# Kernel optimization log

Hardware: AMD Instinct MI355X
Metric: run time of the kernel (lower is better)

Reference implementation:

```python
import jax, jax.numpy as jnp
import numpy as np

N_PARTIAL = 1024  # matches init_kwargs


def setup_inputs() -> dict:
    key = jax.random.key(0)
    k1, k2 = jax.random.split(key)
    B, H, L = 8, 768, 4096
    x = jax.random.normal(k1, (B, H, L), dtype=jnp.float32)
    k = jax.random.normal(k2, (H, L), dtype=jnp.float32)
    return {"x": x, "k": k}


def reference(x, k):
    # FFT-based causal long convolution with low-pass frequency truncation.
    L = x.shape[-1]
    N = 2 * L  # zero-pad to 2L for linear (non-circular) convolution
    x_dtype = x.dtype
    x_f = jnp.fft.rfft(x.astype(jnp.float32), n=N)          # [B, H, N//2+1] complex64
    k_f = jnp.fft.rfft(k.astype(jnp.float32), n=N)          # [H, N//2+1]   complex64
    # zero out all frequency bins >= N_partial // 2 (low-pass truncation of the kernel)
    freqs = jnp.arange(N // 2 + 1)
    k_f = jnp.where(freqs < N_PARTIAL // 2, k_f, jnp.zeros((), dtype=k_f.dtype))
    y_f = x_f * k_f                                          # broadcast over batch
    y = jnp.fft.irfft(y_f, n=N)[..., :L].astype(x_dtype)     # [B, H, L]
    return y
```

## Files before the change

### kernel.cpp

```cpp
#include <hip/hip_runtime.h>
#include <math.h>

#define LSEQ 4096
#define NFFT 8192
#define NF   512
#define NF2  1024
#define NH   768
#define NBH  6144
#define MROWS 6912

typedef __attribute__((ext_vector_type(8))) short short8;
typedef __attribute__((ext_vector_type(4))) float floatx4;

__device__ __forceinline__ unsigned short f2bf(float f) {
    unsigned int u = __float_as_uint(f);
    u += 0x7fff + ((u >> 16) & 1);
    return (unsigned short)(u >> 16);
}

__device__ __forceinline__ void gld16(const unsigned short* g, unsigned short* l) {
    __builtin_amdgcn_global_load_lds(
        (const __attribute__((address_space(1))) void*)g,
        (__attribute__((address_space(3))) void*)l, 16, 0, 0);
}

__global__ void build_tables(unsigned short* __restrict__ T1,
                             unsigned short* __restrict__ T2) {
    __shared__ unsigned short tile[64][66];
    const int t = threadIdx.x;
    const int F0 = blockIdx.x * 64;
    const int N0 = blockIdx.y * 64;
#pragma unroll
    for (int i = 0; i < 16; ++i) {
        int r = (t >> 6) + i * 4;
        int c = t & 63;
        int f2 = F0 + r, n = N0 + c;
        int f = f2 >> 1;
        int p = (f * n) & (NFFT - 1);
        float th = (float)p * (float)(2.0 * M_PI / (double)NFFT);
        float s, cc;
        sincosf(th, &s, &cc);
        unsigned short v = f2bf((f2 & 1) ? s : cc);
        T1[(size_t)f2 * LSEQ + n] = v;
        tile[r][c] = v;
    }
    __syncthreads();
#pragma unroll
    for (int i = 0; i < 16; ++i) {
        int r = (t >> 6) + i * 4;
        int c = t & 63;
        T2[(size_t)(N0 + r) * NF2 + F0 + c] = tile[c][r];
    }
}

__global__ void tobf16(const float* __restrict__ x, const float* __restrict__ kk,
                       unsigned short* __restrict__ o) {
    size_t e = ((size_t)blockIdx.x * 256 + threadIdx.x) * 4;
    const size_t XN = (size_t)NBH * LSEQ;
    const float* s = (e < XN) ? (x + e) : (kk + (e - XN));
    float4 v = *(const float4*)s;
    unsigned int lo = (unsigned int)f2bf(v.x) | ((unsigned int)f2bf(v.y) << 16);
    unsigned int hi = (unsigned int)f2bf(v.z) | ((unsigned int)f2bf(v.w) << 16);
    *(uint2*)(o + e) = make_uint2(lo, hi);
}

__global__ __launch_bounds__(256) void gemm_bt(
    const unsigned short* __restrict__ A,
    const unsigned short* __restrict__ B,
    float* __restrict__ C,
    int M, int N, int K)
{
    __shared__ __align__(16) unsigned short As[2][128 * 32];
    __shared__ __align__(16) unsigned short Bs[2][128 * 32];
    const int t = threadIdx.x;
    const int w = t >> 6, l = t & 63;
    const int m0 = blockIdx.y * 128, n0 = blockIdx.x * 128;
    const int wm = (w >> 1) * 64, wn = (w & 1) * 64;
    const int lq = l >> 4, lr = l & 15;

    floatx4 acc[4][4];
#pragma unroll
    for (int i = 0; i < 4; ++i)
#pragma unroll
        for (int j = 0; j < 4; ++j)
            acc[i][j] = (floatx4){0.f, 0.f, 0.f, 0.f};

    const int sr = l >> 2, se = (l & 3) * 8;
    const int c0 = 2 * w, c1 = 2 * w + 1;
    const unsigned short* gA0 = A + (size_t)(m0 + c0 * 16 + sr) * K + se;
    const unsigned short* gA1 = A + (size_t)(m0 + c1 * 16 + sr) * K + se;
    const unsigned short* gB0 = B + (size_t)(n0 + c0 * 16 + sr) * K + se;
    const unsigned short* gB1 = B + (size_t)(n0 + c1 * 16 + sr) * K + se;

    gld16(gA0, As[0] + c0 * 512);
    gld16(gA1, As[0] + c1 * 512);
    gld16(gB0, Bs[0] + c0 * 512);
    gld16(gB1, Bs[0] + c1 * 512);
    __syncthreads();

    int cur = 0;
    for (int k0 = 32; k0 < K; k0 += 32) {
        const int nxt = cur ^ 1;
        gld16(gA0 + k0, As[nxt] + c0 * 512);
        gld16(gA1 + k0, As[nxt] + c1 * 512);
        gld16(gB0 + k0, Bs[nxt] + c0 * 512);
        gld16(gB1 + k0, Bs[nxt] + c1 * 512);

        short8 af[4], bfv[4];
#pragma unroll
        for (int i = 0; i < 4; ++i)
            af[i] = *(const short8*)(As[cur] + (wm + 16 * i + lr) * 32 + lq * 8);
#pragma unroll
        for (int j = 0; j < 4; ++j)
            bfv[j] = *(const short8*)(Bs[cur] + (wn + 16 * j + lr) * 32 + lq * 8);
#pragma unroll
        for (int i = 0; i < 4; ++i)
#pragma unroll
            for (int j = 0; j < 4; ++j)
                acc[i][j] = __builtin_amdgcn_mfma_f32_16x16x32_bf16(af[i], bfv[j], acc[i][j], 0, 0, 0);

        __syncthreads();
        cur = nxt;
    }

    {
        short8 af[4], bfv[4];
#pragma unroll
        for (int i = 0; i < 4; ++i)
            af[i] = *(const short8*)(As[cur] + (wm + 16 * i + lr) * 32 + lq * 8);
#pragma unroll
        for (int j = 0; j < 4; ++j)
            bfv[j] = *(const short8*)(Bs[cur] + (wn + 16 * j + lr) * 32 + lq * 8);
#pragma unroll
        for (int i = 0; i < 4; ++i)
#pragma unroll
            for (int j = 0; j < 4; ++j)
                acc[i][j] = __builtin_amdgcn_mfma_f32_16x16x32_bf16(af[i], bfv[j], acc[i][j], 0, 0, 0);
    }

#pragma unroll
    for (int i = 0; i < 4; ++i)
#pragma unroll
        for (int j = 0; j < 4; ++j)
#pragma unroll
            for (int r = 0; r < 4; ++r) {
                int row = m0 + wm + 16 * i + lq * 4 + r;
                int col = n0 + wn + 16 * j + lr;
                C[(size_t)row * N + col] = acc[i][j][r];
            }
}

__global__ void combine(const float* __restrict__ C1, unsigned short* __restrict__ AB) {
    int idx = blockIdx.x * blockDim.x + threadIdx.x;
    int bh = idx >> 9;
    int f = idx & (NF - 1);
    int h = bh % NH;
    const float* xc = C1 + (size_t)bh * NF2 + 2 * f;
    const float* kc = C1 + (size_t)(NBH + h) * NF2 + 2 * f;
    float Xre = xc[0], Xim = -xc[1];
    float Kre = kc[0], Kim = -kc[1];
    float s = (f == 0 ? 1.0f : 2.0f) * (1.0f / (float)NFFT);
    float Av = s * (Xre * Kre - Xim * Kim);
    float Bv = -(s * (Xre * Kim + Xim * Kre));
    unsigned int packed = (unsigned int)f2bf(Av) | ((unsigned int)f2bf(Bv) << 16);
    *(unsigned int*)(AB + (size_t)bh * NF2 + 2 * f) = packed;
}

extern "C" void kernel_launch(void* const* d_in, const int* in_sizes, int n_in,
                              void* d_out, int out_size, void* d_ws, size_t ws_size,
                              hipStream_t stream) {
    const float* x = (const float*)d_in[0];
    const float* k = (const float*)d_in[1];
    float* y = (float*)d_out;

    unsigned short* T1 = (unsigned short*)d_ws;
    unsigned short* T2 = T1 + (size_t)NF2 * LSEQ;
    unsigned short* AB = T2 + (size_t)LSEQ * NF2;

    unsigned short* Abm = (unsigned short*)d_out;
    float* C1 = (float*)((char*)d_out + (size_t)MROWS * LSEQ * 2);

    const int blk = 256;
    hipLaunchKernelGGL(build_tables, dim3(NF2 / 64, LSEQ / 64), dim3(blk), 0, stream, T1, T2);
    hipLaunchKernelGGL(tobf16, dim3((MROWS * LSEQ / 4) / blk), dim3(blk), 0, stream, x, k, Abm);
    hipLaunchKernelGGL(gemm_bt, dim3(NF2 / 128, MROWS / 128), dim3(blk), 0, stream,
                       Abm, T1, C1, MROWS, NF2, LSEQ);
    hipLaunchKernelGGL(combine, dim3((NBH * NF) / blk), dim3(blk), 0, stream, C1, AB);
    hipLaunchKernelGGL(gemm_bt, dim3(LSEQ / 128, NBH / 128), dim3(blk), 0, stream,
                       AB, T2, y, NBH, LSEQ, NF2);
}
```

Before: 356.6 us.

## Split-K the forward DFT GEMM and switch to register-staged double buffering

```diff
diff --git a/kernel.cpp b/kernel.cpp
--- a/kernel.cpp
+++ b/kernel.cpp
@@ -8,6 +8,7 @@
 #define NH   768
 #define NBH  6144
 #define MROWS 6912
+#define SPLIT_ROW 3456
 
 typedef __attribute__((ext_vector_type(8))) short short8;
 typedef __attribute__((ext_vector_type(4))) float floatx4;
@@ -16,12 +17,6 @@
     unsigned int u = __float_as_uint(f);
     u += 0x7fff + ((u >> 16) & 1);
     return (unsigned short)(u >> 16);
-}
-
-__device__ __forceinline__ void gld16(const unsigned short* g, unsigned short* l) {
-    __builtin_amdgcn_global_load_lds(
-        (const __attribute__((address_space(1))) void*)g,
-        (__attribute__((address_space(3))) void*)l, 16, 0, 0);
 }
 
 __global__ void build_tables(unsigned short* __restrict__ T1,
@@ -64,11 +59,42 @@
     *(uint2*)(o + e) = make_uint2(lo, hi);
 }
 
+#define LOADSET(ra0, ra1, rb0, rb1, off)                      \
+    ra0 = *(const uint4*)(pa0 + (off));                        \
+    ra1 = *(const uint4*)(pa1 + (off));                        \
+    rb0 = *(const uint4*)(pb0 + (off));                        \
+    rb1 = *(const uint4*)(pb1 + (off));
+
+#define WRITESET(buf, ra0, ra1, rb0, rb1)                      \
+    *(uint4*)(As[buf] + q0 * 8) = ra0;                         \
+    *(uint4*)(As[buf] + q1 * 8) = ra1;                         \
+    *(uint4*)(Bs[buf] + q0 * 8) = rb0;                         \
+    *(uint4*)(Bs[buf] + q1 * 8) = rb1;
+
+#define COMPUTE(buf)                                                          \
+    {                                                                         \
+        short8 af[4], bfv[4];                                                 \
+        _Pragma("unroll")                                                     \
+        for (int i = 0; i < 4; ++i)                                           \
+            af[i] = *(const short8*)(As[buf] + (wm + 16 * i + lr) * 32 + lq * 8); \
+        _Pragma("unroll")                                                     \
+        for (int j = 0; j < 4; ++j)                                           \
+            bfv[j] = *(const short8*)(Bs[buf] + (wn + 16 * j + lr) * 32 + lq * 8); \
+        _Pragma("unroll")                                                     \
+        for (int i = 0; i < 4; ++i)                                           \
+            _Pragma("unroll")                                                 \
+            for (int j = 0; j < 4; ++j)                                       \
+                acc[i][j] = __builtin_amdgcn_mfma_f32_16x16x32_bf16(          \
+                    af[i], bfv[j], acc[i][j], 0, 0, 0);                       \
+    }
+
 __global__ __launch_bounds__(256) void gemm_bt(
     const unsigned short* __restrict__ A,
     const unsigned short* __restrict__ B,
     float* __restrict__ C,
-    int M, int N, int K)
+    float* __restrict__ P1a,
+    float* __restrict__ P1b,
+    int M, int N, int ldk, int Ksub)
 {
     __shared__ __align__(16) unsigned short As[2][128 * 32];
     __shared__ __align__(16) unsigned short Bs[2][128 * 32];
@@ -77,6 +103,7 @@
     const int m0 = blockIdx.y * 128, n0 = blockIdx.x * 128;
     const int wm = (w >> 1) * 64, wn = (w & 1) * 64;
     const int lq = l >> 4, lr = l & 15;
+    const int kbase = blockIdx.z * Ksub;
 
     floatx4 acc[4][4];
 #pragma unroll
@@ -85,59 +112,44 @@
         for (int j = 0; j < 4; ++j)
             acc[i][j] = (floatx4){0.f, 0.f, 0.f, 0.f};
 
-    const int sr = l >> 2, se = (l & 3) * 8;
-    const int c0 = 2 * w, c1 = 2 * w + 1;
-    const unsigned short* gA0 = A + (size_t)(m0 + c0 * 16 + sr) * K + se;
-    const unsigned short* gA1 = A + (size_t)(m0 + c1 * 16 + sr) * K + se;
-    const unsigned short* gB0 = B + (size_t)(n0 + c0 * 16 + sr) * K + se;
-    const unsigned short* gB1 = B + (size_t)(n0 + c1 * 16 + sr) * K + se;
-
-    gld16(gA0, As[0] + c0 * 512);
-    gld16(gA1, As[0] + c1 * 512);
-    gld16(gB0, Bs[0] + c0 * 512);
-    gld16(gB1, Bs[0] + c1 * 512);
+    const int q0 = t, q1 = t + 256;
+    const int r0 = q0 >> 2, e0 = (q0 & 3) * 8;
+    const int r1 = q1 >> 2, e1 = (q1 & 3) * 8;
+    const unsigned short* pa0 = A + (size_t)(m0 + r0) * ldk + e0 + kbase;
+    const unsigned short* pa1 = A + (size_t)(m0 + r1) * ldk + e1 + kbase;
+    const unsigned short* pb0 = B + (size_t)(n0 + r0) * ldk + e0 + kbase;
+    const unsigned short* pb1 = B + (size_t)(n0 + r1) * ldk + e1 + kbase;
+
+    uint4 xa0, xa1, xb0, xb1;
+    uint4 ya0, ya1, yb0, yb1;
+
+    LOADSET(xa0, xa1, xb0, xb1, 0)
+    WRITESET(0, xa0, xa1, xb0, xb1)
+    LOADSET(ya0, ya1, yb0, yb1, 32)
     __syncthreads();
 
-    int cur = 0;
-    for (int k0 = 32; k0 < K; k0 += 32) {
-        const int nxt = cur ^ 1;
-        gld16(gA0 + k0, As[nxt] + c0 * 512);
-        gld16(gA1 + k0, As[nxt] + c1 * 512);
-        gld16(gB0 + k0, Bs[nxt] + c0 * 512);
-        gld16(gB1 + k0, Bs[nxt] + c1 * 512);
-
-        short8 af[4], bfv[4];
-#pragma unroll
-        for (int i = 0; i < 4; ++i)
-            af[i] = *(const short8*)(As[cur] + (wm + 16 * i + lr) * 32 + lq * 8);
-#pragma unroll
-        for (int j = 0; j < 4; ++j)
-            bfv[j] = *(const short8*)(Bs[cur] + (wn + 16 * j + lr) * 32 + lq * 8);
-#pragma unroll
-        for (int i = 0; i < 4; ++i)
-#pragma unroll
-            for (int j = 0; j < 4; ++j)
-                acc[i][j] = __builtin_amdgcn_mfma_f32_16x16x32_bf16(af[i], bfv[j], acc[i][j], 0, 0, 0);
-
+    const int T = Ksub >> 5;
+    for (int tt = 0; tt + 4 <= T; tt += 2) {
+        LOADSET(xa0, xa1, xb0, xb1, (tt + 2) * 32)
+        COMPUTE(0)
+        WRITESET(1, ya0, ya1, yb0, yb1)
         __syncthreads();
-        cur = nxt;
-    }
-
-    {
-        short8 af[4], bfv[4];
-#pragma unroll
-        for (int i = 0; i < 4; ++i)
-            af[i] = *(const short8*)(As[cur] + (wm + 16 * i + lr) * 32 + lq * 8);
-#pragma unroll
-        for (int j = 0; j < 4; ++j)
-            bfv[j] = *(const short8*)(Bs[cur] + (wn + 16 * j + lr) * 32 + lq * 8);
-#pragma unroll
-        for (int i = 0; i < 4; ++i)
-#pragma unroll
-            for (int j = 0; j < 4; ++j)
-                acc[i][j] = __builtin_amdgcn_mfma_f32_16x16x32_bf16(af[i], bfv[j], acc[i][j], 0, 0, 0);
-    }
-
+        LOADSET(ya0, ya1, yb0, yb1, (tt + 3) * 32)
+        COMPUTE(1)
+        WRITESET(0, xa0, xa1, xb0, xb1)
+        __syncthreads();
+    }
+    COMPUTE(0)
+    WRITESET(1, ya0, ya1, yb0, yb1)
+    __syncthreads();
+    COMPUTE(1)
+
+    float* Cb;
+    if (blockIdx.z == 0) {
+        Cb = C;
+    } else {
+        Cb = (m0 < SPLIT_ROW) ? P1a : (P1b - (size_t)SPLIT_ROW * N);
+    }
 #pragma unroll
     for (int i = 0; i < 4; ++i)
 #pragma unroll
@@ -146,19 +158,27 @@
             for (int r = 0; r < 4; ++r) {
                 int row = m0 + wm + 16 * i + lq * 4 + r;
                 int col = n0 + wn + 16 * j + lr;
-                C[(size_t)row * N + col] = acc[i][j][r];
+                Cb[(size_t)row * N + col] = acc[i][j][r];
             }
 }
 
-__global__ void combine(const float* __restrict__ C1, unsigned short* __restrict__ AB) {
+__global__ void combine(const float* __restrict__ C1,
+                        const float* __restrict__ P1a,
+                        const float* __restrict__ P1b,
+                        unsigned short* __restrict__ AB) {
     int idx = blockIdx.x * blockDim.x + threadIdx.x;
     int bh = idx >> 9;
     int f = idx & (NF - 1);
     int h = bh % NH;
     const float* xc = C1 + (size_t)bh * NF2 + 2 * f;
-    const float* kc = C1 + (size_t)(NBH + h) * NF2 + 2 * f;
-    float Xre = xc[0], Xim = -xc[1];
-    float Kre = kc[0], Kim = -kc[1];
+    const float* xp = (bh < SPLIT_ROW)
+        ? (P1a + (size_t)bh * NF2 + 2 * f)
+        : (P1b + (size_t)(bh - SPLIT_ROW) * NF2 + 2 * f);
+    const int kr = NBH + h;
+    const float* kc = C1 + (size_t)kr * NF2 + 2 * f;
+    const float* kp = P1b + (size_t)(kr - SPLIT_ROW) * NF2 + 2 * f;
+    float Xre = xc[0] + xp[0], Xim = -(xc[1] + xp[1]);
+    float Kre = kc[0] + kp[0], Kim = -(kc[1] + kp[1]);
     float s = (f == 0 ? 1.0f : 2.0f) * (1.0f / (float)NFFT);
     float Av = s * (Xre * Kre - Xim * Kim);
     float Bv = -(s * (Xre * Kim + Xim * Kre));
@@ -176,16 +196,18 @@
     unsigned short* T1 = (unsigned short*)d_ws;
     unsigned short* T2 = T1 + (size_t)NF2 * LSEQ;
     unsigned short* AB = T2 + (size_t)LSEQ * NF2;
+    float* P1a = (float*)(AB + (size_t)NBH * NF2);
 
     unsigned short* Abm = (unsigned short*)d_out;
     float* C1 = (float*)((char*)d_out + (size_t)MROWS * LSEQ * 2);
+    float* P1b = C1 + (size_t)MROWS * NF2;
 
     const int blk = 256;
     hipLaunchKernelGGL(build_tables, dim3(NF2 / 64, LSEQ / 64), dim3(blk), 0, stream, T1, T2);
     hipLaunchKernelGGL(tobf16, dim3((MROWS * LSEQ / 4) / blk), dim3(blk), 0, stream, x, k, Abm);
-    hipLaunchKernelGGL(gemm_bt, dim3(NF2 / 128, MROWS / 128), dim3(blk), 0, stream,
-                       Abm, T1, C1, MROWS, NF2, LSEQ);
-    hipLaunchKernelGGL(combine, dim3((NBH * NF) / blk), dim3(blk), 0, stream, C1, AB);
-    hipLaunchKernelGGL(gemm_bt, dim3(LSEQ / 128, NBH / 128), dim3(blk), 0, stream,
-                       AB, T2, y, NBH, LSEQ, NF2);
-}
+    hipLaunchKernelGGL(gemm_bt, dim3(NF2 / 128, MROWS / 128, 2), dim3(blk), 0, stream,
+                       Abm, T1, C1, P1a, P1b, MROWS, NF2, LSEQ, LSEQ / 2);
+    hipLaunchKernelGGL(combine, dim3((NBH * NF) / blk), dim3(blk), 0, stream, C1, P1a, P1b, AB);
+    hipLaunchKernelGGL(gemm_bt, dim3(LSEQ / 128, NBH / 128, 1), dim3(blk), 0, stream,
+                       AB, T2, y, (float*)nullptr, (float*)nullptr, NBH, LSEQ, NF2, NF2);
+}
```

Result: faster. 349.3 us (-2.1%).
